# Kernel tuning notes

Measured on AMD Instinct MI355X. Metric: run time of the kernel, lower is better.

Reference implementation:

```python
import jax, jax.numpy as jnp
import numpy as np

E = 7       # number of experts (len(expert_details))
K = 2       # top-k routing
CAP = 3072  # per-expert capacity ~ ceil(T*K/E * 1.25)
D = 1024    # d_model
H = 4096    # d_ff = 4*d_model
T = 8192    # tokens (B=2, S=4096)


def setup_inputs() -> dict:
    key = jax.random.key(0)
    k1, k2, k3, k4 = jax.random.split(key, 4)
    x = jax.random.normal(k1, (T, D), jnp.float32)
    Wg = jax.random.normal(k2, (D, E), jnp.float32) * 0.02
    W1 = jax.random.normal(k3, (E, D, H), jnp.float32) * 0.02
    W2 = jax.random.normal(k4, (E, H, D), jnp.float32) * 0.02
    return {"x": x, "Wg": Wg, "W1": W1, "W2": W2}


def reference(x, Wg, W1, W2):
    Tn, Dn = x.shape
    # --- router ---
    gates = jax.nn.softmax(x @ Wg, axis=-1)          # [T, E]
    topw, topi = jax.lax.top_k(gates, K)             # [T, K]
    topw = topw / jnp.sum(topw, axis=-1, keepdims=True)
    flat_e = topi.reshape(-1)                        # [T*K] expert ids (int)
    flat_w = topw.reshape(-1)                        # [T*K] combine weights
    # --- position within each expert (priority = token order) ---
    onehot = jax.nn.one_hot(flat_e, E, dtype=jnp.int32)           # [T*K, E]
    pos = jnp.sum(jnp.cumsum(onehot, axis=0) * onehot, axis=-1) - 1  # [T*K]
    keep = pos < CAP
    slot = jnp.where(keep, pos, CAP)  # overflow tokens go to pad slot CAP
    # --- dispatch: scatter tokens into [E, CAP, D] buffer ---
    x_rep = jnp.repeat(x, K, axis=0)                               # [T*K, D]
    buf = jnp.zeros((E, CAP + 1, Dn), x.dtype).at[flat_e, slot].set(x_rep)[:, :CAP]
    # --- grouped expert FFN (grouped GEMMs) ---
    h = jax.nn.gelu(jnp.einsum('ecd,edh->ech', buf, W1))
    y = jnp.einsum('ech,ehd->ecd', h, W2)                          # [E, CAP, D]
    # --- combine: gather back and weight ---
    y_pad = jnp.concatenate([y, jnp.zeros((E, 1, Dn), y.dtype)], axis=1)
    out_slots = y_pad[flat_e, slot] * (flat_w * keep.astype(flat_w.dtype))[:, None]
    return out_slots.reshape(Tn, K, Dn).sum(axis=1)                # [T, D]
```

## Files before the change

kernel.cpp:

```cpp
#include <hip/hip_runtime.h>
#include <stdint.h>


#define NEXP 7
#define KTOP 2
#define CAP 3072
#define DM 1024
#define HF 4096
#define TT 8192

typedef __bf16 bf16x8 __attribute__((ext_vector_type(8)));
typedef float f32x4 __attribute__((ext_vector_type(4)));

__device__ __forceinline__ unsigned short f2bf(float v) {
  union { float f; unsigned u; } a; a.f = v;
  unsigned r = a.u + 0x7FFFu + ((a.u >> 16) & 1u);
  return (unsigned short)(r >> 16);
}
__device__ __forceinline__ float bf2f(unsigned short h) {
  union { unsigned u; float f; } a; a.u = ((unsigned)h) << 16; return a.f;
}
__device__ __forceinline__ float gelu_t(float v) {
  float u = 0.7978845608028654f * (v + 0.044715f * v * v * v);
  float ex = __expf(2.0f * u);
  float th = 1.0f - 2.0f / (ex + 1.0f);
  return 0.5f * v * (1.0f + th);
}
__device__ __forceinline__ void gl2lds16(const void* g, void* l) {
  __builtin_amdgcn_global_load_lds(
      (const __attribute__((address_space(1))) unsigned int*)g,
      (__attribute__((address_space(3))) unsigned int*)l, 16, 0, 0);
}

__global__ void init_counts(int* counts) {
  if (threadIdx.x < NEXP) counts[threadIdx.x] = 0;
}

__global__ void router_kernel(const float* __restrict__ x, const float* __restrict__ Wg,
                              int* __restrict__ counts, int* __restrict__ flatE,
                              int* __restrict__ flatSlot, int* __restrict__ tokOfSlot,
                              float* __restrict__ wOfSlot) {
  int wave = threadIdx.x >> 6, lane = threadIdx.x & 63;
  int t = blockIdx.x * 4 + wave;
  double acc[NEXP];
#pragma unroll
  for (int e = 0; e < NEXP; ++e) acc[e] = 0.0;
  const float* xr = x + (long)t * DM;
  for (int j = 0; j < DM / 64; ++j) {
    int d = j * 64 + lane;
    double xv = (double)xr[d];
#pragma unroll
    for (int e = 0; e < NEXP; ++e) acc[e] += xv * (double)Wg[d * NEXP + e];
  }
#pragma unroll
  for (int e = 0; e < NEXP; ++e) {
#pragma unroll
    for (int off = 32; off > 0; off >>= 1) acc[e] += __shfl_down(acc[e], off);
  }
  if (lane == 0) {
    int i1 = 0; double l1 = acc[0];
    for (int e2 = 1; e2 < NEXP; ++e2) if (acc[e2] > l1) { l1 = acc[e2]; i1 = e2; }
    int i2 = -1; double l2 = -1e300;
    for (int e2 = 0; e2 < NEXP; ++e2) if (e2 != i1 && acc[e2] > l2) { l2 = acc[e2]; i2 = e2; }
    float w1 = (float)(1.0 / (1.0 + exp(l2 - l1)));
    float w2 = 1.0f - w1;
    int fi0 = t * 2, fi1 = t * 2 + 1;
    int p0 = atomicAdd(&counts[i1], 1);
    flatE[fi0] = i1; flatSlot[fi0] = (p0 < CAP) ? p0 : CAP;
    if (p0 < CAP) { tokOfSlot[i1 * CAP + p0] = fi0; wOfSlot[i1 * CAP + p0] = w1; }
    int p1 = atomicAdd(&counts[i2], 1);
    flatE[fi1] = i2; flatSlot[fi1] = (p1 < CAP) ? p1 : CAP;
    if (p1 < CAP) { tokOfSlot[i2 * CAP + p1] = fi1; wOfSlot[i2 * CAP + p1] = w2; }
  }
}

__global__ void transcvt(const float* __restrict__ in, unsigned short* __restrict__ out,
                         int R, int C) {
  __shared__ float tile[64][65];
  long base = (long)blockIdx.z * (long)R * (long)C;
  const float* inp = in + base;
  unsigned short* outp = out + base;
  int c0 = blockIdx.x * 64, r0 = blockIdx.y * 64;
  int lx = threadIdx.x & 63, ly = threadIdx.x >> 6;
#pragma unroll
  for (int i = 0; i < 16; ++i) {
    int r = ly + i * 4;
    tile[r][lx] = inp[(long)(r0 + r) * C + c0 + lx];
  }
  __syncthreads();
#pragma unroll
  for (int i = 0; i < 16; ++i) {
    int c = ly + i * 4;
    outp[(long)(c0 + c) * R + r0 + lx] = f2bf(tile[lx][c]);
  }
}

__global__ void scatter_x(const float* __restrict__ x, const int* __restrict__ flatE,
                          const int* __restrict__ flatSlot, unsigned short* __restrict__ xb) {
  int fi = blockIdx.x;
  int s = flatSlot[fi];
  if (s >= CAP) return;
  int e = flatE[fi];
  const float4* xr = (const float4*)(x + (long)(fi >> 1) * DM);
  float4 v = xr[threadIdx.x];
  ushort4 o; o.x = f2bf(v.x); o.y = f2bf(v.y); o.z = f2bf(v.z); o.w = f2bf(v.w);
  ((ushort4*)(xb + ((long)e * CAP + s) * DM))[threadIdx.x] = o;
}

template <int EPI>
__global__ __launch_bounds__(256, 2) void gemm_bt(
    const unsigned short* __restrict__ A, const unsigned short* __restrict__ Bt,
    void* __restrict__ Cout, const int* __restrict__ counts,
    const int* __restrict__ tokOfSlot, const float* __restrict__ wOfSlot,
    int K, int N, int eoff, long aexps, long cexps) {
  __shared__ unsigned short sA[128 * 32];
  __shared__ unsigned short sB[128 * 32];
  int e = eoff + blockIdx.z;
  int mcnt = counts[e]; mcnt = mcnt < CAP ? mcnt : CAP;
  int m0 = blockIdx.y * 128;
  if (m0 >= mcnt) return;
  int n0 = blockIdx.x * 128;
  const unsigned short* Ae = A + (long)blockIdx.z * aexps;
  const unsigned short* Be = Bt + (long)e * (long)N * (long)K;

  int tid = threadIdx.x;
  int lane = tid & 63, wave = tid >> 6;
  int lm = lane & 15, quad = lane >> 4;
  int wm = (wave & 1) * 64, wn = (wave >> 1) * 64;

  int ra = tid >> 2;
  int ca = (tid & 3) * 8;
  const unsigned short* Ab0 = Ae + (long)(m0 + ra) * K + ca;
  const unsigned short* Ab1 = Ae + (long)(m0 + 64 + ra) * K + ca;
  const unsigned short* Bb0 = Be + (long)(n0 + ra) * K + ca;
  const unsigned short* Bb1 = Be + (long)(n0 + 64 + ra) * K + ca;
  unsigned short* sAp0 = &sA[tid * 8];
  unsigned short* sAp1 = &sA[(tid + 256) * 8];
  unsigned short* sBp0 = &sB[tid * 8];
  unsigned short* sBp1 = &sB[(tid + 256) * 8];

  f32x4 acc[4][4];
#pragma unroll
  for (int i = 0; i < 4; ++i)
#pragma unroll
    for (int j = 0; j < 4; ++j) acc[i][j] = f32x4{0.f, 0.f, 0.f, 0.f};

  for (int k0 = 0; k0 < K; k0 += 32) {
    gl2lds16(Ab0 + k0, sAp0);
    gl2lds16(Ab1 + k0, sAp1);
    gl2lds16(Bb0 + k0, sBp0);
    gl2lds16(Bb1 + k0, sBp1);
    __syncthreads();
    bf16x8 aF[4], bF[4];
#pragma unroll
    for (int mi = 0; mi < 4; ++mi)
      aF[mi] = *(const bf16x8*)&sA[(wm + mi * 16 + lm) * 32 + quad * 8];
#pragma unroll
    for (int ni = 0; ni < 4; ++ni)
      bF[ni] = *(const bf16x8*)&sB[(wn + ni * 16 + lm) * 32 + quad * 8];
#pragma unroll
    for (int mi = 0; mi < 4; ++mi)
#pragma unroll
      for (int ni = 0; ni < 4; ++ni)
        acc[mi][ni] = __builtin_amdgcn_mfma_f32_16x16x32_bf16(aF[mi], bF[ni], acc[mi][ni], 0, 0, 0);
    __syncthreads();
  }

  if (EPI == 0) {
    unsigned short* Ce = (unsigned short*)Cout + (long)blockIdx.z * cexps;
#pragma unroll
    for (int mi = 0; mi < 4; ++mi) {
      int mb = m0 + wm + mi * 16 + quad * 4;
#pragma unroll
      for (int r = 0; r < 4; ++r) {
        int m = mb + r;
        if (m < mcnt) {
#pragma unroll
          for (int ni = 0; ni < 4; ++ni) {
            int n = n0 + wn + ni * 16 + lm;
            Ce[(long)m * N + n] = f2bf(gelu_t(acc[mi][ni][r]));
          }
        }
      }
    }
  } else {
    unsigned short* Y = (unsigned short*)Cout;
#pragma unroll
    for (int mi = 0; mi < 4; ++mi) {
      int mb = m0 + wm + mi * 16 + quad * 4;
#pragma unroll
      for (int r = 0; r < 4; ++r) {
        int m = mb + r;
        if (m < mcnt) {
          int fi = tokOfSlot[e * CAP + m];
          float w = wOfSlot[e * CAP + m];
#pragma unroll
          for (int ni = 0; ni < 4; ++ni) {
            int n = n0 + wn + ni * 16 + lm;
            Y[(long)fi * N + n] = f2bf(w * acc[mi][ni][r]);
          }
        }
      }
    }
  }
}

__global__ void combine_k(const unsigned short* __restrict__ yflat,
                          const int* __restrict__ flatSlot, float* __restrict__ out) {
  int t = blockIdx.x;
  bool k0 = flatSlot[2 * t] < CAP, k1 = flatSlot[2 * t + 1] < CAP;
  const ushort4* y0 = (const ushort4*)(yflat + (long)(2 * t) * DM);
  const ushort4* y1 = (const ushort4*)(yflat + (long)(2 * t + 1) * DM);
  ushort4 a = y0[threadIdx.x], b = y1[threadIdx.x];
  float4 r;
  r.x = (k0 ? bf2f(a.x) : 0.f) + (k1 ? bf2f(b.x) : 0.f);
  r.y = (k0 ? bf2f(a.y) : 0.f) + (k1 ? bf2f(b.y) : 0.f);
  r.z = (k0 ? bf2f(a.z) : 0.f) + (k1 ? bf2f(b.z) : 0.f);
  r.w = (k0 ? bf2f(a.w) : 0.f) + (k1 ? bf2f(b.w) : 0.f);
  ((float4*)(out + (long)t * DM))[threadIdx.x] = r;
}

extern "C" void kernel_launch(void* const* d_in, const int* in_sizes, int n_in,
                              void* d_out, int out_size, void* d_ws, size_t ws_size,
                              hipStream_t stream) {
  const float* x  = (const float*)d_in[0];
  const float* Wg = (const float*)d_in[1];
  const float* W1 = (const float*)d_in[2];
  const float* W2 = (const float*)d_in[3];
  float* out = (float*)d_out;

  char* ws = (char*)d_ws;
  size_t off = 0;
  auto alloc = [&](size_t b) { void* p = ws + off; off = (off + b + 255) & ~(size_t)255; return p; };
  int* counts            = (int*)alloc(NEXP * 4);
  int* flatE             = (int*)alloc((size_t)TT * KTOP * 4);
  int* flatSlot          = (int*)alloc((size_t)TT * KTOP * 4);
  int* tokOfSlot         = (int*)alloc((size_t)NEXP * CAP * 4);
  float* wOfSlot         = (float*)alloc((size_t)NEXP * CAP * 4);
  unsigned short* Wb1    = (unsigned short*)alloc((size_t)NEXP * DM * HF * 2);
  unsigned short* Wb2    = (unsigned short*)alloc((size_t)NEXP * DM * HF * 2);
  unsigned short* xb     = (unsigned short*)alloc((size_t)NEXP * CAP * DM * 2);
  unsigned short* yflat  = (unsigned short*)alloc((size_t)TT * KTOP * DM * 2);
  size_t hbA = (size_t)NEXP * CAP * HF * 2;
  size_t hbB = (size_t)CAP * HF * 2;
  int planA = (off + hbA) <= ws_size;
  unsigned short* hb = (unsigned short*)alloc(planA ? hbA : hbB);

  init_counts<<<1, 64, 0, stream>>>(counts);
  router_kernel<<<TT / 4, 256, 0, stream>>>(x, Wg, counts, flatE, flatSlot, tokOfSlot, wOfSlot);
  transcvt<<<dim3(HF / 64, DM / 64, NEXP), 256, 0, stream>>>(W1, Wb1, DM, HF);
  transcvt<<<dim3(DM / 64, HF / 64, NEXP), 256, 0, stream>>>(W2, Wb2, HF, DM);
  scatter_x<<<TT * KTOP, 256, 0, stream>>>(x, flatE, flatSlot, xb);

  if (planA) {
    gemm_bt<0><<<dim3(HF / 128, CAP / 128, NEXP), 256, 0, stream>>>(
        xb, Wb1, hb, counts, tokOfSlot, wOfSlot, DM, HF, 0, (long)CAP * DM, (long)CAP * HF);
    gemm_bt<1><<<dim3(DM / 128, CAP / 128, NEXP), 256, 0, stream>>>(
        hb, Wb2, yflat, counts, tokOfSlot, wOfSlot, HF, DM, 0, (long)CAP * HF, 0);
  } else {
    for (int e = 0; e < NEXP; ++e) {
      gemm_bt<0><<<dim3(HF / 128, CAP / 128, 1), 256, 0, stream>>>(
          xb + (size_t)e * CAP * DM, Wb1, hb, counts, tokOfSlot, wOfSlot, DM, HF, e, 0, 0);
      gemm_bt<1><<<dim3(DM / 128, CAP / 128, 1), 256, 0, stream>>>(
          hb, Wb2, yflat, counts, tokOfSlot, wOfSlot, HF, DM, e, 0, 0);
    }
  }
  combine_k<<<TT, 256, 0, stream>>>(yflat, flatSlot, out);
}
```

Before: 947.4 us.

## Add 256x256 double-buffered swizzled GEMM with split-K for second expert GEMM

Replaces the 128x128 single-stage grouped GEMMs with a new 512-thread kernel. It uses 256x256 tiles, 64-wide K steps, XOR-swizzled LDS layout, and double-buffered global-to-LDS loads interleaved with MFMA phases using setprio and explicit waitcnt. The second GEMM is split along K into two halves written to separate partial buffers, and a new combine kernel sums them. This targets better data reuse and latency hiding, at the cost of doubling the yflat workspace and larger per-block LDS and register use.

```diff
diff --git a/kernel.cpp b/kernel.cpp
--- a/kernel.cpp
+++ b/kernel.cpp
@@ -105,6 +105,155 @@
   float4 v = xr[threadIdx.x];
   ushort4 o; o.x = f2bf(v.x); o.y = f2bf(v.y); o.z = f2bf(v.z); o.w = f2bf(v.w);
   ((ushort4*)(xb + ((long)e * CAP + s) * DM))[threadIdx.x] = o;
+}
+
+template <int EPI>
+__global__ __launch_bounds__(512, 2) void gemm256(
+    const unsigned short* __restrict__ A, const unsigned short* __restrict__ Bt,
+    void* __restrict__ Cout, const int* __restrict__ counts,
+    const int* __restrict__ tokOfSlot, const float* __restrict__ wOfSlot,
+    int LD, int klen, int N, int kspl, long aexps, long cexps) {
+  __shared__ __align__(16) unsigned short sAb[2][16384];
+  __shared__ __align__(16) unsigned short sBb[2][16384];
+  int e = blockIdx.z / kspl, ks = blockIdx.z % kspl;
+  int mcnt = counts[e]; mcnt = mcnt < CAP ? mcnt : CAP;
+  int m0 = blockIdx.y * 256;
+  if (m0 >= mcnt) return;
+  int n0 = blockIdx.x * 256;
+  long kstart = (long)ks * klen;
+
+  const unsigned short* Ae = A + (long)e * aexps;
+  const unsigned short* Be = Bt + (long)e * (long)N * LD;
+
+  int tid = threadIdx.x;
+  int lane = tid & 63, wave = tid >> 6;
+  int wr = wave >> 2, wc = wave & 3;
+  int lm = lane & 15, quad = lane >> 4;
+
+  int srow = tid >> 3;
+  int scol = ((lane & 7) ^ (lane >> 3)) << 3;
+  const unsigned short* As = Ae + (long)(m0 + srow) * LD + kstart + scol;
+  const unsigned short* Bs = Be + (long)(n0 + srow) * LD + kstart + scol;
+
+  int abase = (wr * 128 + lm) * 64;
+  int bbase = (wc * 64 + lm) * 64;
+  int cx0 = (quad ^ (lm & 7)) << 3;
+  int cx1 = ((quad + 4) ^ (lm & 7)) << 3;
+
+  f32x4 acc[8][4];
+#pragma unroll
+  for (int i = 0; i < 8; ++i)
+#pragma unroll
+    for (int j = 0; j < 4; ++j) acc[i][j] = f32x4{0.f, 0.f, 0.f, 0.f};
+
+  int NT = klen >> 6, NI = NT >> 1;
+
+#define STA(buf, kt, half) do { \
+    int _kt = (kt) < NT ? (kt) : (NT - 1); \
+    gl2lds16(As + (long)_kt * 64 + (long)((half) * 2) * 64 * LD, \
+             &sAb[buf][(half) * 8192 + tid * 8]); \
+    gl2lds16(As + (long)_kt * 64 + (long)((half) * 2 + 1) * 64 * LD, \
+             &sAb[buf][(half) * 8192 + 4096 + tid * 8]); \
+  } while (0)
+#define STB(buf, kt, half) do { \
+    int _kt = (kt) < NT ? (kt) : (NT - 1); \
+    gl2lds16(Bs + (long)_kt * 64 + (long)((half) * 2) * 64 * LD, \
+             &sBb[buf][(half) * 8192 + tid * 8]); \
+    gl2lds16(Bs + (long)_kt * 64 + (long)((half) * 2 + 1) * 64 * LD, \
+             &sBb[buf][(half) * 8192 + 4096 + tid * 8]); \
+  } while (0)
+
+  bf16x8 bF[4][2];
+
+#define PHASE(buf, mi0, RB, STAGE, VM) do { \
+    bf16x8 a00 = *(const bf16x8*)&sAb[buf][abase + (mi0) * 1024 + cx0]; \
+    bf16x8 a01 = *(const bf16x8*)&sAb[buf][abase + (mi0) * 1024 + cx1]; \
+    bf16x8 a10 = *(const bf16x8*)&sAb[buf][abase + (mi0) * 1024 + 1024 + cx0]; \
+    bf16x8 a11 = *(const bf16x8*)&sAb[buf][abase + (mi0) * 1024 + 1024 + cx1]; \
+    if (RB) { \
+      _Pragma("unroll") \
+      for (int ni = 0; ni < 4; ++ni) { \
+        bF[ni][0] = *(const bf16x8*)&sBb[buf][bbase + ni * 1024 + cx0]; \
+        bF[ni][1] = *(const bf16x8*)&sBb[buf][bbase + ni * 1024 + cx1]; \
+      } \
+    } \
+    STAGE; \
+    __builtin_amdgcn_s_barrier(); \
+    asm volatile("s_waitcnt lgkmcnt(0)" ::: "memory"); \
+    __builtin_amdgcn_sched_barrier(0); \
+    __builtin_amdgcn_s_setprio(1); \
+    _Pragma("unroll") \
+    for (int ni = 0; ni < 4; ++ni) { \
+      acc[mi0][ni]     = __builtin_amdgcn_mfma_f32_16x16x32_bf16(a00, bF[ni][0], acc[mi0][ni], 0, 0, 0); \
+      acc[mi0][ni]     = __builtin_amdgcn_mfma_f32_16x16x32_bf16(a01, bF[ni][1], acc[mi0][ni], 0, 0, 0); \
+      acc[mi0 + 1][ni] = __builtin_amdgcn_mfma_f32_16x16x32_bf16(a10, bF[ni][0], acc[mi0 + 1][ni], 0, 0, 0); \
+      acc[mi0 + 1][ni] = __builtin_amdgcn_mfma_f32_16x16x32_bf16(a11, bF[ni][1], acc[mi0 + 1][ni], 0, 0, 0); \
+    } \
+    __builtin_amdgcn_s_setprio(0); \
+    VM; \
+    __builtin_amdgcn_s_barrier(); \
+  } while (0)
+
+  STA(0, 0, 0); STA(0, 0, 1); STB(0, 0, 0); STB(0, 0, 1);
+  STB(1, 1, 0); STB(1, 1, 1);
+  asm volatile("s_waitcnt vmcnt(4)" ::: "memory");
+  __builtin_amdgcn_s_barrier();
+
+  for (int t = 0; t < NI; ++t) {
+    int k0 = 2 * t, k1 = 2 * t + 1;
+    PHASE(0, 0, 1, STA(1, k1, 0), (void)0);
+    PHASE(0, 2, 0, STA(1, k1, 1), (void)0);
+    PHASE(0, 4, 0, STB(0, k0 + 2, 0), (void)0);
+    PHASE(0, 6, 0, STB(0, k0 + 2, 1),
+          asm volatile("s_waitcnt vmcnt(4)" ::: "memory"));
+    PHASE(1, 0, 1, STA(0, k0 + 2, 0), (void)0);
+    PHASE(1, 2, 0, STA(0, k0 + 2, 1), (void)0);
+    PHASE(1, 4, 0, STB(1, k1 + 2, 0), (void)0);
+    PHASE(1, 6, 0, STB(1, k1 + 2, 1),
+          asm volatile("s_waitcnt vmcnt(4)" ::: "memory"));
+  }
+  asm volatile("s_waitcnt vmcnt(0)" ::: "memory");
+#undef PHASE
+#undef STA
+#undef STB
+
+  if (EPI == 0) {
+    unsigned short* Ce = (unsigned short*)Cout + (long)e * cexps;
+#pragma unroll
+    for (int mi = 0; mi < 8; ++mi) {
+      int mb = m0 + wr * 128 + mi * 16 + quad * 4;
+#pragma unroll
+      for (int r = 0; r < 4; ++r) {
+        int m = mb + r;
+        if (m < mcnt) {
+#pragma unroll
+          for (int ni = 0; ni < 4; ++ni) {
+            int n = n0 + wc * 64 + ni * 16 + lm;
+            Ce[(long)m * N + n] = f2bf(gelu_t(acc[mi][ni][r]));
+          }
+        }
+      }
+    }
+  } else {
+    unsigned short* Y = (unsigned short*)Cout + (long)ks * ((long)TT * KTOP * DM);
+#pragma unroll
+    for (int mi = 0; mi < 8; ++mi) {
+      int mb = m0 + wr * 128 + mi * 16 + quad * 4;
+#pragma unroll
+      for (int r = 0; r < 4; ++r) {
+        int m = mb + r;
+        if (m < mcnt) {
+          int fi = tokOfSlot[e * CAP + m];
+          float w = wOfSlot[e * CAP + m];
+#pragma unroll
+          for (int ni = 0; ni < 4; ++ni) {
+            int n = n0 + wc * 64 + ni * 16 + lm;
+            Y[(long)fi * N + n] = f2bf(w * acc[mi][ni][r]);
+          }
+        }
+      }
+    }
+  }
 }
 
 template <int EPI>
@@ -151,18 +300,18 @@
     gl2lds16(Bb0 + k0, sBp0);
     gl2lds16(Bb1 + k0, sBp1);
     __syncthreads();
-    bf16x8 aF[4], bF[4];
+    bf16x8 aF[4], bFf[4];
 #pragma unroll
     for (int mi = 0; mi < 4; ++mi)
       aF[mi] = *(const bf16x8*)&sA[(wm + mi * 16 + lm) * 32 + quad * 8];
 #pragma unroll
     for (int ni = 0; ni < 4; ++ni)
-      bF[ni] = *(const bf16x8*)&sB[(wn + ni * 16 + lm) * 32 + quad * 8];
+      bFf[ni] = *(const bf16x8*)&sB[(wn + ni * 16 + lm) * 32 + quad * 8];
 #pragma unroll
     for (int mi = 0; mi < 4; ++mi)
 #pragma unroll
       for (int ni = 0; ni < 4; ++ni)
-        acc[mi][ni] = __builtin_amdgcn_mfma_f32_16x16x32_bf16(aF[mi], bF[ni], acc[mi][ni], 0, 0, 0);
+        acc[mi][ni] = __builtin_amdgcn_mfma_f32_16x16x32_bf16(aF[mi], bFf[ni], acc[mi][ni], 0, 0, 0);
     __syncthreads();
   }
 
@@ -203,6 +352,25 @@
       }
     }
   }
+}
+
+__global__ void combine_k2(const unsigned short* __restrict__ yflat,
+                           const int* __restrict__ flatSlot, float* __restrict__ out) {
+  int t = blockIdx.x;
+  bool k0 = flatSlot[2 * t] < CAP, k1 = flatSlot[2 * t + 1] < CAP;
+  const long S = (long)TT * KTOP * DM;
+  const ushort4* y00 = (const ushort4*)(yflat + (long)(2 * t) * DM);
+  const ushort4* y01 = (const ushort4*)(yflat + S + (long)(2 * t) * DM);
+  const ushort4* y10 = (const ushort4*)(yflat + (long)(2 * t + 1) * DM);
+  const ushort4* y11 = (const ushort4*)(yflat + S + (long)(2 * t + 1) * DM);
+  ushort4 a = y00[threadIdx.x], a2 = y01[threadIdx.x];
+  ushort4 b = y10[threadIdx.x], b2 = y11[threadIdx.x];
+  float4 r;
+  r.x = (k0 ? bf2f(a.x) + bf2f(a2.x) : 0.f) + (k1 ? bf2f(b.x) + bf2f(b2.x) : 0.f);
+  r.y = (k0 ? bf2f(a.y) + bf2f(a2.y) : 0.f) + (k1 ? bf2f(b.y) + bf2f(b2.y) : 0.f);
+  r.z = (k0 ? bf2f(a.z) + bf2f(a2.z) : 0.f) + (k1 ? bf2f(b.z) + bf2f(b2.z) : 0.f);
+  r.w = (k0 ? bf2f(a.w) + bf2f(a2.w) : 0.f) + (k1 ? bf2f(b.w) + bf2f(b2.w) : 0.f);
+  ((float4*)(out + (long)t * DM))[threadIdx.x] = r;
 }
 
 __global__ void combine_k(const unsigned short* __restrict__ yflat,
@@ -240,7 +408,7 @@
   unsigned short* Wb1    = (unsigned short*)alloc((size_t)NEXP * DM * HF * 2);
   unsigned short* Wb2    = (unsigned short*)alloc((size_t)NEXP * DM * HF * 2);
   unsigned short* xb     = (unsigned short*)alloc((size_t)NEXP * CAP * DM * 2);
-  unsigned short* yflat  = (unsigned short*)alloc((size_t)TT * KTOP * DM * 2);
+  unsigned short* yflat  = (unsigned short*)alloc((size_t)2 * TT * KTOP * DM * 2);
   size_t hbA = (size_t)NEXP * CAP * HF * 2;
   size_t hbB = (size_t)CAP * HF * 2;
   int planA = (off + hbA) <= ws_size;
@@ -253,10 +421,13 @@
   scatter_x<<<TT * KTOP, 256, 0, stream>>>(x, flatE, flatSlot, xb);
 
   if (planA) {
-    gemm_bt<0><<<dim3(HF / 128, CAP / 128, NEXP), 256, 0, stream>>>(
-        xb, Wb1, hb, counts, tokOfSlot, wOfSlot, DM, HF, 0, (long)CAP * DM, (long)CAP * HF);
-    gemm_bt<1><<<dim3(DM / 128, CAP / 128, NEXP), 256, 0, stream>>>(
-        hb, Wb2, yflat, counts, tokOfSlot, wOfSlot, HF, DM, 0, (long)CAP * HF, 0);
+    gemm256<0><<<dim3(HF / 256, CAP / 256, NEXP), 512, 0, stream>>>(
+        xb, Wb1, hb, counts, tokOfSlot, wOfSlot, DM, DM, HF, 1,
+        (long)CAP * DM, (long)CAP * HF);
+    gemm256<1><<<dim3(DM / 256, CAP / 256, NEXP * 2), 512, 0, stream>>>(
+        hb, Wb2, yflat, counts, tokOfSlot, wOfSlot, HF, HF / 2, DM, 2,
+        (long)CAP * HF, 0);
+    combine_k2<<<TT, 256, 0, stream>>>(yflat, flatSlot, out);
   } else {
     for (int e = 0; e < NEXP; ++e) {
       gemm_bt<0><<<dim3(HF / 128, CAP / 128, 1), 256, 0, stream>>>(
@@ -264,6 +435,6 @@
       gemm_bt<1><<<dim3(DM / 128, CAP / 128, 1), 256, 0, stream>>>(
           hb, Wb2, yflat, counts, tokOfSlot, wOfSlot, HF, DM, e, 0, 0);
     }
-  }
-  combine_k<<<TT, 256, 0, stream>>>(yflat, flatSlot, out);
-}
+    combine_k<<<TT, 256, 0, stream>>>(yflat, flatSlot, out);
+  }
+}
```

Measured after the change: 930.7 us. No clear change (-1.8%).
